# Kernel tuning notes

Measured on AMD Instinct MI355X. Metric: run time of the kernel, lower is better.

Reference implementation:

```python
import jax, jax.numpy as jnp
import numpy as np

B, C_IN, C_OUT, H, W = 128, 128, 128, 40, 40
NUM_EXPERTS, TOP_K, EXPAND = 8, 2, 2
C_HID = C_IN * EXPAND


def setup_inputs() -> dict:
    key = jax.random.key(0)
    ks = jax.random.split(key, 6)
    x = jax.random.normal(ks[0], (B, C_IN, H, W), dtype=jnp.float32)
    weights = jax.random.uniform(ks[1], (B, TOP_K), dtype=jnp.float32)
    indices = jax.random.randint(ks[2], (B, TOP_K), 0, NUM_EXPERTS, dtype=jnp.int64)
    # per-expert 1x1 conv params: expand -> SiLU -> project
    W1 = jax.random.normal(ks[3], (NUM_EXPERTS, C_HID, C_IN), dtype=jnp.float32) * (1.0 / np.sqrt(C_IN))
    b1 = jnp.zeros((NUM_EXPERTS, C_HID), dtype=jnp.float32)
    W2 = jax.random.normal(ks[4], (NUM_EXPERTS, C_OUT, C_HID), dtype=jnp.float32) * (1.0 / np.sqrt(C_HID))
    b2 = jnp.zeros((NUM_EXPERTS, C_OUT), dtype=jnp.float32)
    return {"x": x, "weights": weights, "indices": indices,
            "W1": W1, "b1": b1, "W2": W2, "b2": b2}


def reference(x, weights, indices, W1, b1, W2, b2):
    # Combine top-k gate weights per (batch, expert): duplicate expert picks sum,
    # exactly matching the original's per-expert gather + weighted index_add_.
    Bn = x.shape[0]
    E = W1.shape[0]
    gate = jnp.zeros((Bn, E), dtype=x.dtype).at[jnp.arange(Bn)[:, None], indices].add(weights)  # [B, E]
    out = jnp.zeros((Bn, W2.shape[1]) + x.shape[2:], dtype=x.dtype)
    for e in range(E):  # fixed small expert loop
        h = jax.nn.silu(jnp.einsum('bchw,oc->bohw', x, W1[e]) + b1[e][None, :, None, None])
        y = jnp.einsum('bchw,oc->bohw', h, W2[e]) + b2[e][None, :, None, None]
        out = out + y * gate[:, e][:, None, None, None]
    return out
```

## Files before the change

### kernel.cpp

```cpp
#include <hip/hip_runtime.h>

#define CIN   128
#define CHID  256
#define COUT  128
#define HWPX  1600
#define PXW   64
#define NPXT  25

typedef __attribute__((ext_vector_type(8))) short bf16x8;
typedef __attribute__((ext_vector_type(4))) float f32x4;

__device__ __forceinline__ unsigned short f2bf(float f) {
  unsigned int u = __builtin_bit_cast(unsigned int, f);
  u += 0x7FFFu + ((u >> 16) & 1u);
  return (unsigned short)(u >> 16);
}

__device__ __forceinline__ unsigned int pack_bf2(float a, float b) {
  return (unsigned int)f2bf(a) | ((unsigned int)f2bf(b) << 16);
}

__device__ __forceinline__ unsigned int silu_gate_pk(float a, float b, float g) {
  const float sa = g * a / (1.0f + __expf(-a));
  const float sb = g * b / (1.0f + __expf(-b));
  return pack_bf2(sa, sb);
}

__global__ __launch_bounds__(256) void convert_w_kernel(
    const float* __restrict__ W1, const float* __restrict__ W2,
    unsigned short* __restrict__ W1b, unsigned short* __restrict__ W2b) {
  int i = blockIdx.x * 256 + threadIdx.x;
  W2b[i] = f2bf(W2[i]);
  int c = i % CIN;
  int p = (i / CIN) % CHID;
  int e = i / (CIN * CHID);
  int g  = p >> 5;
  int pp = p & 31;
  int mt = pp >> 4;
  int row = pp & 15;
  int ch = (g << 5) + ((row >> 2) << 3) + (row & 3) + (mt << 2);
  W1b[i] = f2bf(W1[(e * CHID + ch) * CIN + c]);
}

__global__ __launch_bounds__(64, 2) void moe_kernel(
    const float* __restrict__ x, const float* __restrict__ wts,
    const int* __restrict__ idx, const unsigned short* __restrict__ W1,
    const float* __restrict__ b1, const unsigned short* __restrict__ W2,
    const float* __restrict__ b2, float* __restrict__ out) {
  __shared__ unsigned short xs[PXW][CIN + 8];

  const int lane = threadIdx.x;
  const int q    = lane >> 4;
  const int r16  = lane & 15;

  const int blk = blockIdx.x;
  const int b   = blk / NPXT;
  const int pt  = blk - b * NPXT;
  const int px0 = pt * PXW;

  {
    const float* xb = x + (long)b * CIN * HWPX + px0 + lane;
#pragma unroll
    for (int c8 = 0; c8 < 16; ++c8) {
      const int c0 = c8 * 8;
      float v[8];
#pragma unroll
      for (int j = 0; j < 8; ++j) v[j] = xb[(long)(c0 + j) * HWPX];
      union { bf16x8 w; unsigned int u[4]; } t;
#pragma unroll
      for (int d = 0; d < 4; ++d)
        t.u[d] = pack_bf2(v[2 * d], v[2 * d + 1]);
      *reinterpret_cast<bf16x8*>(&xs[lane][c0]) = t.w;
    }
  }
  __syncthreads();

  bf16x8 xpin[2][4];
#pragma unroll
  for (int ks = 0; ks < 2; ++ks)
#pragma unroll
    for (int nt = 0; nt < 4; ++nt)
      xpin[ks][nt] = *reinterpret_cast<const bf16x8*>(
          &xs[nt * 16 + r16][ks * 32 + q * 8]);

  f32x4 accO[8][4];
#pragma unroll
  for (int mt = 0; mt < 8; ++mt)
#pragma unroll
    for (int nt = 0; nt < 4; ++nt) accO[mt][nt] = (f32x4){0.f, 0.f, 0.f, 0.f};

  const int   e0 = idx[b * 2 + 0], e1 = idx[b * 2 + 1];
  const float g0 = wts[b * 2 + 0], g1 = wts[b * 2 + 1];

  for (int slot = 0; slot < 2; ++slot) {
    const int   e = slot ? e1 : e0;
    const float g = slot ? g1 : g0;
    const unsigned short* W1e = W1 + (long)e * CHID * CIN;
    const unsigned short* W2e = W2 + (long)e * COUT * CHID;
    const float* b1e = b1 + e * CHID;

    for (int grp = 0; grp < 8; ++grp) {
      const int base = grp * 32;

      f32x4 aA[4], aB[4];
#pragma unroll
      for (int nt = 0; nt < 4; ++nt) {
        aA[nt] = (f32x4){0.f, 0.f, 0.f, 0.f};
        aB[nt] = (f32x4){0.f, 0.f, 0.f, 0.f};
      }
#pragma unroll
      for (int ks = 0; ks < 4; ++ks) {
        const bf16x8 w0 = *reinterpret_cast<const bf16x8*>(
            W1e + (base + r16) * CIN + ks * 32 + q * 8);
        const bf16x8 w1 = *reinterpret_cast<const bf16x8*>(
            W1e + (base + 16 + r16) * CIN + ks * 32 + q * 8);
        bf16x8 xf[4];
#pragma unroll
        for (int nt = 0; nt < 4; ++nt) {
          if (ks < 2)
            xf[nt] = xpin[ks][nt];
          else
            xf[nt] = *reinterpret_cast<const bf16x8*>(
                &xs[nt * 16 + r16][ks * 32 + q * 8]);
        }
#pragma unroll
        for (int nt = 0; nt < 4; ++nt) {
          aA[nt] = __builtin_amdgcn_mfma_f32_16x16x32_bf16(w0, xf[nt], aA[nt], 0, 0, 0);
          aB[nt] = __builtin_amdgcn_mfma_f32_16x16x32_bf16(w1, xf[nt], aB[nt], 0, 0, 0);
        }
      }

      const f32x4 bA = *reinterpret_cast<const f32x4*>(&b1e[base + q * 8]);
      const f32x4 bB = *reinterpret_cast<const f32x4*>(&b1e[base + q * 8 + 4]);
      union { bf16x8 v; unsigned int u[4]; } h[4];
#pragma unroll
      for (int nt = 0; nt < 4; ++nt) {
        h[nt].u[0] = silu_gate_pk(aA[nt][0] + bA[0], aA[nt][1] + bA[1], g);
        h[nt].u[1] = silu_gate_pk(aA[nt][2] + bA[2], aA[nt][3] + bA[3], g);
        h[nt].u[2] = silu_gate_pk(aB[nt][0] + bB[0], aB[nt][1] + bB[1], g);
        h[nt].u[3] = silu_gate_pk(aB[nt][2] + bB[2], aB[nt][3] + bB[3], g);
      }

#pragma unroll
      for (int mt = 0; mt < 8; ++mt) {
        const bf16x8 w2 = *reinterpret_cast<const bf16x8*>(
            W2e + (mt * 16 + r16) * CHID + base + q * 8);
#pragma unroll
        for (int nt = 0; nt < 4; ++nt)
          accO[mt][nt] = __builtin_amdgcn_mfma_f32_16x16x32_bf16(w2, h[nt].v, accO[mt][nt], 0, 0, 0);
      }
    }
  }

  const float* b2e0 = b2 + e0 * COUT;
  const float* b2e1 = b2 + e1 * COUT;
  const long ob = (long)b * COUT * HWPX + px0 + r16;
#pragma unroll
  for (int mt = 0; mt < 8; ++mt) {
    const int co = mt * 16 + q * 4;
    const f32x4 bias = g0 * (*reinterpret_cast<const f32x4*>(&b2e0[co])) +
                       g1 * (*reinterpret_cast<const f32x4*>(&b2e1[co]));
#pragma unroll
    for (int nt = 0; nt < 4; ++nt) {
      const f32x4 v = accO[mt][nt] + bias;
#pragma unroll
      for (int r = 0; r < 4; ++r)
        out[ob + (long)(co + r) * HWPX + nt * 16] = v[r];
    }
  }
}

extern "C" void kernel_launch(void* const* d_in, const int* in_sizes, int n_in,
                              void* d_out, int out_size, void* d_ws, size_t ws_size,
                              hipStream_t stream) {
  const float* x   = (const float*)d_in[0];
  const float* wts = (const float*)d_in[1];
  const int*   idx = (const int*)d_in[2];
  const float* W1  = (const float*)d_in[3];
  const float* b1  = (const float*)d_in[4];
  const float* W2  = (const float*)d_in[5];
  const float* b2  = (const float*)d_in[6];
  float* out = (float*)d_out;

  unsigned short* W1b = (unsigned short*)d_ws;
  unsigned short* W2b = (unsigned short*)d_ws + (8 * CHID * CIN);

  convert_w_kernel<<<262144 / 256, 256, 0, stream>>>(W1, W2, W1b, W2b);
  moe_kernel<<<128 * NPXT, 64, 0, stream>>>(x, wts, idx, W1b, b1, W2b, b2, out);
}
```

Measured before the change: 338.1 us.

## Share expert weights in LDS across four waves with prefetch and swizzled layout

Each block now runs four waves, each handling one 64-pixel tile of the same batch. The block stages each 32-channel group of W1/W2 into LDS once and shares it across the waves, prefetching the next group into registers while the current one computes. Both the weight and activation LDS layouts are XOR-style swizzled to avoid bank conflicts. Output goes through an LDS staging buffer so stores are coalesced float4 writes. The cost is extra barriers per group and idle waves in the last partial block (25 tiles over 7×4 slots).

After: 302.8 us. 1.12x faster.

```diff
diff --git a/kernel.cpp b/kernel.cpp
--- a/kernel.cpp
+++ b/kernel.cpp
@@ -4,8 +4,6 @@
 #define CHID  256
 #define COUT  128
 #define HWPX  1600
-#define PXW   64
-#define NPXT  25
 
 typedef __attribute__((ext_vector_type(8))) short bf16x8;
 typedef __attribute__((ext_vector_type(4))) float f32x4;
@@ -15,11 +13,9 @@
   u += 0x7FFFu + ((u >> 16) & 1u);
   return (unsigned short)(u >> 16);
 }
-
 __device__ __forceinline__ unsigned int pack_bf2(float a, float b) {
   return (unsigned int)f2bf(a) | ((unsigned int)f2bf(b) << 16);
 }
-
 __device__ __forceinline__ unsigned int silu_gate_pk(float a, float b, float g) {
   const float sa = g * a / (1.0f + __expf(-a));
   const float sb = g * b / (1.0f + __expf(-b));
@@ -29,143 +25,175 @@
 __global__ __launch_bounds__(256) void convert_w_kernel(
     const float* __restrict__ W1, const float* __restrict__ W2,
     unsigned short* __restrict__ W1b, unsigned short* __restrict__ W2b) {
-  int i = blockIdx.x * 256 + threadIdx.x;
-  W2b[i] = f2bf(W2[i]);
-  int c = i % CIN;
-  int p = (i / CIN) % CHID;
-  int e = i / (CIN * CHID);
-  int g  = p >> 5;
-  int pp = p & 31;
-  int mt = pp >> 4;
-  int row = pp & 15;
-  int ch = (g << 5) + ((row >> 2) << 3) + (row & 3) + (mt << 2);
-  W1b[i] = f2bf(W1[(e * CHID + ch) * CIN + c]);
-}
-
-__global__ __launch_bounds__(64, 2) void moe_kernel(
+  const int i   = blockIdx.x * 256 + threadIdx.x;
+  const int j   = i & 7;
+  const int p   = (i >> 3) & 511;
+  const int grp = (i >> 12) & 7;
+  const int e   = i >> 15;
+  {
+    const int r   = p >> 4;
+    const int c   = ((p & 15) - r) & 15;
+    const int row = r & 15, mt = r >> 4;
+    const int ch  = grp * 32 + ((row >> 2) << 3) + (row & 3) + (mt << 2);
+    W1b[i] = f2bf(W1[(e * CHID + ch) * CIN + c * 8 + j]);
+  }
+  {
+    const int co = p >> 2;
+    const int c  = ((p & 3) - co - (co >> 2)) & 3;
+    const int ch = grp * 32 + c * 8 + j;
+    W2b[i] = f2bf(W2[(e * COUT + co) * CHID + ch]);
+  }
+}
+
+__global__ __launch_bounds__(256, 2) void moe_kernel(
     const float* __restrict__ x, const float* __restrict__ wts,
     const int* __restrict__ idx, const unsigned short* __restrict__ W1,
     const float* __restrict__ b1, const unsigned short* __restrict__ W2,
     const float* __restrict__ b2, float* __restrict__ out) {
-  __shared__ unsigned short xs[PXW][CIN + 8];
-
-  const int lane = threadIdx.x;
+  __shared__ __align__(16) unsigned short lds[40960];
+
+  const int tid  = threadIdx.x;
+  const int wave = tid >> 6;
+  const int lane = tid & 63;
   const int q    = lane >> 4;
   const int r16  = lane & 15;
 
-  const int blk = blockIdx.x;
-  const int b   = blk / NPXT;
-  const int pt  = blk - b * NPXT;
-  const int px0 = pt * PXW;
+  const int  b     = blockIdx.x / 7;
+  const int  t4    = blockIdx.x % 7;
+  const int  tile  = t4 * 4 + wave;
+  const bool valid = (tile < 25);
+  const int  tileC = valid ? tile : 24;
+  const int  px0   = tileC * 64;
+
+  unsigned short* xw = &lds[wave * 8192];
 
   {
     const float* xb = x + (long)b * CIN * HWPX + px0 + lane;
-#pragma unroll
-    for (int c8 = 0; c8 < 16; ++c8) {
-      const int c0 = c8 * 8;
+#pragma unroll 4
+    for (int c = 0; c < 16; ++c) {
       float v[8];
 #pragma unroll
-      for (int j = 0; j < 8; ++j) v[j] = xb[(long)(c0 + j) * HWPX];
+      for (int jj = 0; jj < 8; ++jj) v[jj] = xb[(long)(c * 8 + jj) * HWPX];
       union { bf16x8 w; unsigned int u[4]; } t;
 #pragma unroll
-      for (int d = 0; d < 4; ++d)
-        t.u[d] = pack_bf2(v[2 * d], v[2 * d + 1]);
-      *reinterpret_cast<bf16x8*>(&xs[lane][c0]) = t.w;
-    }
-  }
-  __syncthreads();
-
-  bf16x8 xpin[2][4];
-#pragma unroll
-  for (int ks = 0; ks < 2; ++ks)
-#pragma unroll
-    for (int nt = 0; nt < 4; ++nt)
-      xpin[ks][nt] = *reinterpret_cast<const bf16x8*>(
-          &xs[nt * 16 + r16][ks * 32 + q * 8]);
-
-  f32x4 accO[8][4];
-#pragma unroll
-  for (int mt = 0; mt < 8; ++mt)
-#pragma unroll
-    for (int nt = 0; nt < 4; ++nt) accO[mt][nt] = (f32x4){0.f, 0.f, 0.f, 0.f};
+      for (int d = 0; d < 4; ++d) t.u[d] = pack_bf2(v[2 * d], v[2 * d + 1]);
+      const int slot = (c + lane) & 15;
+      *reinterpret_cast<bf16x8*>(&xw[(lane * 16 + slot) * 8]) = t.w;
+    }
+  }
 
   const int   e0 = idx[b * 2 + 0], e1 = idx[b * 2 + 1];
   const float g0 = wts[b * 2 + 0], g1 = wts[b * 2 + 1];
 
-  for (int slot = 0; slot < 2; ++slot) {
-    const int   e = slot ? e1 : e0;
-    const float g = slot ? g1 : g0;
-    const unsigned short* W1e = W1 + (long)e * CHID * CIN;
-    const unsigned short* W2e = W2 + (long)e * COUT * CHID;
-    const float* b1e = b1 + e * CHID;
-
-    for (int grp = 0; grp < 8; ++grp) {
-      const int base = grp * 32;
-
-      f32x4 aA[4], aB[4];
+  f32x4 accO[8][4];
+#pragma unroll
+  for (int mt = 0; mt < 8; ++mt)
+#pragma unroll
+    for (int nt = 0; nt < 4; ++nt) accO[mt][nt] = (f32x4){0.f, 0.f, 0.f, 0.f};
+
+  const uint4* w1g = reinterpret_cast<const uint4*>(W1);
+  const uint4* w2g = reinterpret_cast<const uint4*>(W2);
+  uint4* ws1 = reinterpret_cast<uint4*>(&lds[32768]);
+  uint4* ws2 = reinterpret_cast<uint4*>(&lds[36864]);
+
+  uint4 p1a, p1b, p2a, p2b;
+  {
+    const long base = (long)e0 * 4096 + tid;
+    p1a = w1g[base]; p1b = w1g[base + 256];
+    p2a = w2g[base]; p2b = w2g[base + 256];
+  }
+
+  for (int gs = 0; gs < 16; ++gs) {
+    const int   slot = gs >> 3;
+    const int   grp  = gs & 7;
+    const int   e    = slot ? e1 : e0;
+    const float g    = slot ? g1 : g0;
+
+    __syncthreads();
+    ws1[tid] = p1a; ws1[tid + 256] = p1b;
+    ws2[tid] = p2a; ws2[tid + 256] = p2b;
+    __syncthreads();
+
+    if (gs < 15) {
+      const int  gs2  = gs + 1;
+      const int  e2   = (gs2 >> 3) ? e1 : e0;
+      const long base = (long)e2 * 4096 + (long)(gs2 & 7) * 512 + tid;
+      p1a = w1g[base]; p1b = w1g[base + 256];
+      p2a = w2g[base]; p2b = w2g[base + 256];
+    }
+
+    f32x4 aA[4], aB[4];
+#pragma unroll
+    for (int nt = 0; nt < 4; ++nt) {
+      aA[nt] = (f32x4){0.f, 0.f, 0.f, 0.f};
+      aB[nt] = (f32x4){0.f, 0.f, 0.f, 0.f};
+    }
+#pragma unroll
+    for (int ks = 0; ks < 4; ++ks) {
+      const int slotw = (ks * 4 + q + r16) & 15;
+      const bf16x8 w0 = *reinterpret_cast<const bf16x8*>(
+          &lds[32768 + (r16 * 16 + slotw) * 8]);
+      const bf16x8 w1v = *reinterpret_cast<const bf16x8*>(
+          &lds[32768 + ((r16 + 16) * 16 + slotw) * 8]);
 #pragma unroll
       for (int nt = 0; nt < 4; ++nt) {
-        aA[nt] = (f32x4){0.f, 0.f, 0.f, 0.f};
-        aB[nt] = (f32x4){0.f, 0.f, 0.f, 0.f};
+        const int px = nt * 16 + r16;
+        const bf16x8 xf = *reinterpret_cast<const bf16x8*>(
+            &xw[(px * 16 + ((ks * 4 + q + px) & 15)) * 8]);
+        aA[nt] = __builtin_amdgcn_mfma_f32_16x16x32_bf16(w0, xf, aA[nt], 0, 0, 0);
+        aB[nt] = __builtin_amdgcn_mfma_f32_16x16x32_bf16(w1v, xf, aB[nt], 0, 0, 0);
       }
-#pragma unroll
-      for (int ks = 0; ks < 4; ++ks) {
-        const bf16x8 w0 = *reinterpret_cast<const bf16x8*>(
-            W1e + (base + r16) * CIN + ks * 32 + q * 8);
-        const bf16x8 w1 = *reinterpret_cast<const bf16x8*>(
-            W1e + (base + 16 + r16) * CIN + ks * 32 + q * 8);
-        bf16x8 xf[4];
-#pragma unroll
-        for (int nt = 0; nt < 4; ++nt) {
-          if (ks < 2)
-            xf[nt] = xpin[ks][nt];
-          else
-            xf[nt] = *reinterpret_cast<const bf16x8*>(
-                &xs[nt * 16 + r16][ks * 32 + q * 8]);
-        }
-#pragma unroll
-        for (int nt = 0; nt < 4; ++nt) {
-          aA[nt] = __builtin_amdgcn_mfma_f32_16x16x32_bf16(w0, xf[nt], aA[nt], 0, 0, 0);
-          aB[nt] = __builtin_amdgcn_mfma_f32_16x16x32_bf16(w1, xf[nt], aB[nt], 0, 0, 0);
-        }
-      }
-
-      const f32x4 bA = *reinterpret_cast<const f32x4*>(&b1e[base + q * 8]);
-      const f32x4 bB = *reinterpret_cast<const f32x4*>(&b1e[base + q * 8 + 4]);
-      union { bf16x8 v; unsigned int u[4]; } h[4];
-#pragma unroll
-      for (int nt = 0; nt < 4; ++nt) {
-        h[nt].u[0] = silu_gate_pk(aA[nt][0] + bA[0], aA[nt][1] + bA[1], g);
-        h[nt].u[1] = silu_gate_pk(aA[nt][2] + bA[2], aA[nt][3] + bA[3], g);
-        h[nt].u[2] = silu_gate_pk(aB[nt][0] + bB[0], aB[nt][1] + bB[1], g);
-        h[nt].u[3] = silu_gate_pk(aB[nt][2] + bB[2], aB[nt][3] + bB[3], g);
-      }
-
-#pragma unroll
-      for (int mt = 0; mt < 8; ++mt) {
-        const bf16x8 w2 = *reinterpret_cast<const bf16x8*>(
-            W2e + (mt * 16 + r16) * CHID + base + q * 8);
-#pragma unroll
-        for (int nt = 0; nt < 4; ++nt)
-          accO[mt][nt] = __builtin_amdgcn_mfma_f32_16x16x32_bf16(w2, h[nt].v, accO[mt][nt], 0, 0, 0);
-      }
-    }
-  }
-
+    }
+
+    const float* b1e = b1 + e * CHID + grp * 32;
+    const f32x4 bA = *reinterpret_cast<const f32x4*>(&b1e[q * 8]);
+    const f32x4 bB = *reinterpret_cast<const f32x4*>(&b1e[q * 8 + 4]);
+    union { bf16x8 v; unsigned int u[4]; } h[4];
+#pragma unroll
+    for (int nt = 0; nt < 4; ++nt) {
+      h[nt].u[0] = silu_gate_pk(aA[nt][0] + bA[0], aA[nt][1] + bA[1], g);
+      h[nt].u[1] = silu_gate_pk(aA[nt][2] + bA[2], aA[nt][3] + bA[3], g);
+      h[nt].u[2] = silu_gate_pk(aB[nt][0] + bB[0], aB[nt][1] + bB[1], g);
+      h[nt].u[3] = silu_gate_pk(aB[nt][2] + bB[2], aB[nt][3] + bB[3], g);
+    }
+
+#pragma unroll
+    for (int mt = 0; mt < 8; ++mt) {
+      const int co = mt * 16 + r16;
+      const bf16x8 w2v = *reinterpret_cast<const bf16x8*>(
+          &lds[36864 + (co * 4 + ((q + co + (co >> 2)) & 3)) * 8]);
+#pragma unroll
+      for (int nt = 0; nt < 4; ++nt)
+        accO[mt][nt] = __builtin_amdgcn_mfma_f32_16x16x32_bf16(w2v, h[nt].v, accO[mt][nt], 0, 0, 0);
+    }
+  }
+
+  float* eb = reinterpret_cast<float*>(xw);
   const float* b2e0 = b2 + e0 * COUT;
   const float* b2e1 = b2 + e1 * COUT;
-  const long ob = (long)b * COUT * HWPX + px0 + r16;
+  const int  coR   = lane >> 2;
+  const int  qtr   = lane & 3;
+  const long orow0 = (long)b * COUT * HWPX + px0 + qtr * 16;
 #pragma unroll
   for (int mt = 0; mt < 8; ++mt) {
-    const int co = mt * 16 + q * 4;
-    const f32x4 bias = g0 * (*reinterpret_cast<const f32x4*>(&b2e0[co])) +
-                       g1 * (*reinterpret_cast<const f32x4*>(&b2e1[co]));
+    const int coW = q * 4;
+    const f32x4 bias = g0 * (*reinterpret_cast<const f32x4*>(&b2e0[mt * 16 + coW])) +
+                       g1 * (*reinterpret_cast<const f32x4*>(&b2e1[mt * 16 + coW]));
 #pragma unroll
     for (int nt = 0; nt < 4; ++nt) {
       const f32x4 v = accO[mt][nt] + bias;
 #pragma unroll
-      for (int r = 0; r < 4; ++r)
-        out[ob + (long)(co + r) * HWPX + nt * 16] = v[r];
+      for (int rr = 0; rr < 4; ++rr)
+        eb[(coW + rr) * 68 + nt * 16 + r16] = v[rr];
+    }
+    if (valid) {
+      const long orow = orow0 + (long)(mt * 16 + coR) * HWPX;
+#pragma unroll
+      for (int i4 = 0; i4 < 4; ++i4) {
+        const float4 ov = *reinterpret_cast<const float4*>(
+            &eb[coR * 68 + qtr * 16 + i4 * 4]);
+        *reinterpret_cast<float4*>(&out[orow + i4 * 4]) = ov;
+      }
     }
   }
 }
@@ -186,5 +214,5 @@
   unsigned short* W2b = (unsigned short*)d_ws + (8 * CHID * CIN);
 
   convert_w_kernel<<<262144 / 256, 256, 0, stream>>>(W1, W2, W1b, W2b);
-  moe_kernel<<<128 * NPXT, 64, 0, stream>>>(x, wts, idx, W1b, b1, W2b, b2, out);
-}
+  moe_kernel<<<128 * 7, 256, 0, stream>>>(x, wts, idx, W1b, b1, W2b, b2, out);
+}
```
